# Kernel tuning notes

Hardware: AMD Instinct MI355X
Metric: run time of the kernel (lower is better)

The kernel has to match this reference:

```python
import jax, jax.numpy as jnp
import numpy as np

C1 = 0.01 ** 2
C2 = 0.03 ** 2
IN_CH = 3
WIN = 11
LEVELS = 5


def _gauss_kernel(k=WIN, sigma=1.5, c=IN_CH):
    ax = np.arange(k, dtype=np.float32) - (k - 1) / 2.0
    g = np.exp(-(ax ** 2) / (2.0 * sigma ** 2))
    g = g / g.sum()
    w2d = np.outer(g, g).astype(np.float32)  # [k,k]
    return jnp.asarray(np.tile(w2d[None, None], (c, 1, 1, 1)))  # [C,1,k,k]


def _dwconv(x, w):
    # depthwise (grouped) conv, 'same' padding for odd kernel
    pad = (w.shape[-1] - 1) // 2
    return jax.lax.conv_general_dilated(
        x, w, window_strides=(1, 1), padding=[(pad, pad), (pad, pad)],
        feature_group_count=x.shape[1],
        dimension_numbers=("NCHW", "OIHW", "NCHW"))


def _ssim_loss(i1, i2, w):
    m1 = _dwconv(i1, w)
    m2 = _dwconv(i2, w)
    m1sq = m1 * m1
    m2sq = m2 * m2
    m12 = m1 * m2
    s1 = _dwconv(i1 * i1, w) - m1sq
    s2 = _dwconv(i2 * i2, w) - m2sq
    s12 = _dwconv(i1 * i2, w) - m12
    ssim = (2 * m12 + C1) * (2 * s12 + C2) / ((m1sq + m2sq + C1) * (s1 + s2 + C2))
    return 1.0 - ssim.mean()


def _avg_pool2(x):
    B, C, H, W = x.shape
    return x.reshape(B, C, H // 2, 2, W // 2, 2).mean(axis=(3, 5))


def setup_inputs() -> dict:
    key = jax.random.key(0)
    k1, k2 = jax.random.split(key)
    img1 = jax.random.uniform(k1, (16, IN_CH, 512, 512), dtype=jnp.float32)
    img2 = jax.random.uniform(k2, (16, IN_CH, 512, 512), dtype=jnp.float32)
    inp = {"img1": img1, "img2": img2}
    for i in range(LEVELS):
        inp[f"g{i}"] = _gauss_kernel()
    return inp


def reference(img1, img2, g0, g1, g2, g3, g4):
    loss = jnp.asarray(0.0, dtype=img1.dtype)
    for w in (g0, g1, g2, g3, g4):
        loss = loss + _ssim_loss(img1, img2, w)
        img1 = _avg_pool2(img1)
        img2 = _avg_pool2(img2)
    return loss
```

## Files before the change

kernel.cpp:

```cpp
#include <hip/hip_runtime.h>
#include <math.h>

#define WIN 11
#define PAD 5
#define TW 64

typedef float v2f __attribute__((ext_vector_type(2)));

struct GW { float g[WIN]; };

template<bool EMIT>
__device__ __forceinline__ float ssim_wave_tile(
    const float* __restrict__ p1, const float* __restrict__ p2,
    int W, int X0, int Y0, const GW& gw, float2* __restrict__ rb,
    float* __restrict__ o1a, float* __restrict__ o1b, int Wout)
{
    const int TH = 32;
    const int lane = threadIdx.x & 63;
    const int gx = X0 + lane;
    const bool cval = gx < W;
    const int hx   = (lane < 5) ? (X0 - 5 + lane) : (X0 + 59 + lane);
    const bool hval = (lane < 10) && ((unsigned)hx < (unsigned)W);
    const int hpos = (lane < 5) ? lane : (64 + lane);
    const int cpos = 5 + lane;
    const int gxc = cval ? gx : 0;
    const int hxc = hval ? hx : gxc;
    const int wpos = (lane < 10) ? hpos : cpos;

    float vMp[11], vSp[11], vMq[11], vSq[11];
#pragma unroll
    for (int k = 0; k < 11; ++k) { vMp[k] = 0.f; vSp[k] = 0.f; vMq[k] = 0.f; vSq[k] = 0.f; }

    float part = 0.f;
    float pprev = 0.f, qprev = 0.f;

    auto LOAD = [&](int t, float& oa, float& ob, float& oah, float& obh) {
        int y = Y0 - PAD + t;
        bool yin = (unsigned)y < (unsigned)W;
        const float* r1 = p1 + (size_t)(yin ? y : 0) * W;
        const float* r2 = p2 + (size_t)(yin ? y : 0) * W;
        float va = r1[gxc], vb = r2[gxc];
        float wa = r1[hxc], wb = r2[hxc];
        bool cv = yin && cval;
        bool hv = yin && hval;
        oa  = cv ? va : 0.f;
        ob  = cv ? vb : 0.f;
        oah = hv ? wa : 0.f;
        obh = hv ? wb : 0.f;
    };

    float a0, b0, ah0, bh0;
    float a1, b1, ah1, bh1;
    LOAD(0, a0, b0, ah0, bh0);
    LOAD(1, a1, b1, ah1, bh1);

#pragma unroll 1
    for (int blk = 0; blk < 4; ++blk) {
#pragma unroll
        for (int u = 0; u < 11; ++u) {
            const int t = blk * 11 + u;

            float a2, b2, ah2, bh2;
            LOAD(t + 2, a2, b2, ah2, bh2);

            float p = a0 + b0, q = a0 - b0;
            float ph = ah0 + bh0, qh = ah0 - bh0;
            rb[cpos] = make_float2(p, q);
            rb[wpos] = (lane < 10) ? make_float2(ph, qh) : make_float2(p, q);
            __builtin_amdgcn_wave_barrier();

            v2f hM = {0.f, 0.f}, hS = {0.f, 0.f};
#pragma unroll
            for (int j = 0; j < WIN; ++j) {
                float2 v = rb[lane + j];
                v2f vm = { v.x, v.y };
                v2f g2 = { gw.g[j], gw.g[j] };
                hM = __builtin_elementwise_fma(g2, vm, hM);
                hS = __builtin_elementwise_fma(g2, vm * vm, hS);
            }
            __builtin_amdgcn_wave_barrier();
            float hp = hM.x, hq = hM.y, hpp = hS.x, hqq = hS.y;

#pragma unroll
            for (int s = 0; s < 11; ++s) {
                const int widx = 10 - ((s - u + 11) % 11);
                float g = gw.g[widx];
                vMp[s] = fmaf(g, hp,  vMp[s]);
                vSp[s] = fmaf(g, hpp, vSp[s]);
                vMq[s] = fmaf(g, hq,  vMq[s]);
                vSq[s] = fmaf(g, hqq, vSq[s]);
            }

            if (EMIT) {
                if (t >= 6 && t <= TH + 4 && (t & 1) == 0) {
                    float sp_ = p + pprev, sq_ = q + qprev;
                    float sp2 = sp_ + __shfl_down(sp_, 1, 64);
                    float sq2 = sq_ + __shfl_down(sq_, 1, 64);
                    if ((lane & 1) == 0) {
                        float P = sp2 * 0.25f, Q = sq2 * 0.25f;
                        int yo = (t - 6) >> 1;
                        size_t oo = (size_t)((Y0 >> 1) + yo) * Wout + ((X0 >> 1) + (lane >> 1));
                        o1a[oo] = (P + Q) * 0.5f;
                        o1b[oo] = (P - Q) * 0.5f;
                    }
                }
                pprev = p; qprev = q;
            }

            {
                int o = t - 10;
                if ((unsigned)o < (unsigned)TH) {
                    bool yok = (unsigned)(Y0 + o) < (unsigned)W;
                    float Mp = vMp[u], Sp_ = vSp[u], Mq = vMq[u], Sq_ = vSq[u];
                    const float C1v = 1e-4f, C2v = 9e-4f;
                    float A = Mp * Mp, B = Mq * Mq;
                    float ABp = A + B, ABm = A - B;
                    float SSp = Sp_ + Sq_, SSm = Sp_ - Sq_;
                    float n1 = fmaf(0.5f, ABm, C1v);
                    float n2 = fmaf(0.5f, SSm - ABm, C2v);
                    float e1 = fmaf(0.5f, ABp, C1v);
                    float e2 = fmaf(0.5f, SSp - ABp, C2v);
                    float v = (n1 * n2) * __builtin_amdgcn_rcpf(e1 * e2);
                    part += (cval && yok) ? v : 0.f;
                }
                vMp[u] = 0.f; vSp[u] = 0.f; vMq[u] = 0.f; vSq[u] = 0.f;
            }

            a0 = a1; b0 = b1; ah0 = ah1; bh0 = bh1;
            a1 = a2; b1 = b2; ah1 = ah2; bh1 = bh2;

            __builtin_amdgcn_sched_barrier(0);
        }
    }

    return part;
}

__global__ __launch_bounds__(256, 4) void ssim_l0_kernel(
    const float* __restrict__ i1, const float* __restrict__ i2,
    float* __restrict__ a1, float* __restrict__ b1,
    double* __restrict__ acc, GW gw)
{
    __shared__ float2 rbs[4][80];
    const int wid = threadIdx.x >> 6;
    const int w = blockIdx.x * 4 + wid;
    const int img = w >> 7;
    const int tt = w & 127;
    const int tx = tt & 7, ty = tt >> 3;
    const size_t off  = (size_t)img * 512 * 512;
    const size_t ooff = (size_t)img * 256 * 256;

    float part = ssim_wave_tile<true>(i1 + off, i2 + off, 512, tx * 64, ty * 32,
                                      gw, rbs[wid], a1 + ooff, b1 + ooff, 256);
#pragma unroll
    for (int o = 32; o > 0; o >>= 1) part += __shfl_down(part, o, 64);
    if ((threadIdx.x & 63) == 0) atomicAdd(acc, (double)part);
}

__global__ __launch_bounds__(256, 4) void ssim_rest_kernel(
    const float* __restrict__ a1, const float* __restrict__ b1,
    const float* __restrict__ a2, const float* __restrict__ b2,
    const float* __restrict__ a3, const float* __restrict__ b3,
    const float* __restrict__ a4, const float* __restrict__ b4,
    double* __restrict__ acc, GW gw)
{
    __shared__ float2 rbs[4][80];
    const int wid = threadIdx.x >> 6;
    const int w = blockIdx.x * 4 + wid;
    const int img = w / 43;
    const int r = w - img * 43;
    int lvl, tx, ty;
    if (r < 32)      { lvl = 1; tx = r & 3;  ty = r >> 2; }
    else if (r < 40) { lvl = 2; int s = r - 32; tx = s & 1; ty = s >> 1; }
    else if (r < 42) { lvl = 3; tx = 0; ty = r - 40; }
    else             { lvl = 4; tx = 0; ty = 0; }
    const int W = 512 >> lvl;
    const float* p1; const float* p2;
    switch (lvl) {
      case 1:  p1 = a1; p2 = b1; break;
      case 2:  p1 = a2; p2 = b2; break;
      case 3:  p1 = a3; p2 = b3; break;
      default: p1 = a4; p2 = b4; break;
    }
    const size_t off = (size_t)img * W * W;

    float part = ssim_wave_tile<false>(p1 + off, p2 + off, W, tx * 64, ty * 32,
                                       gw, rbs[wid], nullptr, nullptr, 0);
#pragma unroll
    for (int o = 32; o > 0; o >>= 1) part += __shfl_down(part, o, 64);
    if ((threadIdx.x & 63) == 0) atomicAdd(acc + lvl, (double)part);
}

__global__ __launch_bounds__(256) void pool_rest_kernel(
    const float* __restrict__ a1, const float* __restrict__ b1,
    float* __restrict__ a2, float* __restrict__ b2,
    float* __restrict__ a3, float* __restrict__ b3,
    float* __restrict__ a4, float* __restrict__ b4)
{
    __shared__ float l2[32][33];
    __shared__ float l3[16][17];
    const int tid = threadIdx.x;
    const int im = blockIdx.y;
    const int tb = blockIdx.x;
    const int tx = tb & 3, ty = tb >> 2;
    const bool second = im >= 48;
    const int ii = second ? im - 48 : im;
    const float* src = (second ? b1 : a1) + (size_t)ii * 256 * 256;
    float* o2 = (second ? b2 : a2) + (size_t)ii * 128 * 128;
    float* o3 = (second ? b3 : a3) + (size_t)ii * 64 * 64;
    float* o4 = (second ? b4 : a4) + (size_t)ii * 32 * 32;
    const int X0 = tx * 64, Y0 = ty * 64;

#pragma unroll
    for (int k = 0; k < 2; ++k) {
        int idx = tid + k * 256;
        int xp = idx & 15;
        int yo = idx >> 4;
        const float* rp = src + (size_t)(Y0 + 2 * yo) * 256 + (X0 + 4 * xp);
        float4 r0 = *(const float4*)rp;
        float4 r1 = *(const float4*)(rp + 256);
        float v0 = (r0.x + r0.y + r1.x + r1.y) * 0.25f;
        float v1 = (r0.z + r0.w + r1.z + r1.w) * 0.25f;
        l2[yo][2 * xp]     = v0;
        l2[yo][2 * xp + 1] = v1;
        float2* op = (float2*)(o2 + (size_t)((Y0 >> 1) + yo) * 128 + ((X0 >> 1) + 2 * xp));
        *op = make_float2(v0, v1);
    }
    __syncthreads();
    {
        int xo = tid & 15, yo = tid >> 4;
        if (yo < 16) {
            float v = (l2[2*yo][2*xo] + l2[2*yo][2*xo+1] +
                       l2[2*yo+1][2*xo] + l2[2*yo+1][2*xo+1]) * 0.25f;
            l3[yo][xo] = v;
            o3[(size_t)((Y0 >> 2) + yo) * 64 + ((X0 >> 2) + xo)] = v;
        }
    }
    __syncthreads();
    if (tid < 64) {
        int xo = tid & 7, yo = tid >> 3;
        float v = (l3[2*yo][2*xo] + l3[2*yo][2*xo+1] +
                   l3[2*yo+1][2*xo] + l3[2*yo+1][2*xo+1]) * 0.25f;
        o4[(size_t)((Y0 >> 3) + yo) * 32 + ((X0 >> 3) + xo)] = v;
    }
}

__global__ void final_kernel(const double* __restrict__ acc, float* __restrict__ out)
{
    double loss = 0.0;
#pragma unroll
    for (int l = 0; l < 5; ++l) {
        double cnt = 48.0 * (double)(512 >> l) * (double)(512 >> l);
        loss += 1.0 - acc[l] / cnt;
    }
    out[0] = (float)loss;
}

extern "C" void kernel_launch(void* const* d_in, const int* in_sizes, int n_in,
                              void* d_out, int out_size, void* d_ws, size_t ws_size,
                              hipStream_t stream)
{
    const float* img1 = (const float*)d_in[0];
    const float* img2 = (const float*)d_in[1];
    float* out = (float*)d_out;

    GW gw;
    double gs[WIN], sum = 0.0;
    for (int i = 0; i < WIN; ++i) {
        double ax = (double)i - 5.0;
        gs[i] = exp(-(ax * ax) / 4.5);
        sum += gs[i];
    }
    for (int i = 0; i < WIN; ++i) gw.g[i] = (float)(gs[i] / sum);

    double* acc = (double*)d_ws;
    float* base = (float*)((char*)d_ws + 64);
    const size_t n1 = 48ull * 256 * 256;
    const size_t n2 = 48ull * 128 * 128;
    const size_t n3 = 48ull * 64 * 64;
    const size_t n4 = 48ull * 32 * 32;
    float* a1 = base;      float* b1 = a1 + n1;
    float* a2 = b1 + n1;   float* b2 = a2 + n2;
    float* a3 = b2 + n2;   float* b3 = a3 + n3;
    float* a4 = b3 + n3;   float* b4 = a4 + n4;

    hipMemsetAsync(acc, 0, 5 * sizeof(double), stream);

    hipLaunchKernelGGL(ssim_l0_kernel, dim3(1536), dim3(256), 0, stream,
                       img1, img2, a1, b1, acc, gw);

    hipLaunchKernelGGL(pool_rest_kernel, dim3(16, 96), dim3(256), 0, stream,
                       a1, b1, a2, b2, a3, b3, a4, b4);

    hipLaunchKernelGGL(ssim_rest_kernel, dim3(516), dim3(256), 0, stream,
                       a1, b1, a2, b2, a3, b3, a4, b4, acc, gw);

    hipLaunchKernelGGL(final_kernel, dim3(1), dim3(1), 0, stream, acc, out);
}
```

Baseline: 263.1 us.

## Double-buffer LDS row buffer and software-pipeline horizontal pass one row ahead

Splits the per-wave LDS row buffer into two halves so the horizontal Gaussian pass for row t reads one buffer while row t+2's sums are written to the other. The LDS reads are issued at the top of the iteration, ahead of the vertical accumulation, and the global load prefetch distance grows from 2 rows to 4. The goal is to hide LDS and global load latency behind the vertical FMA chain and to drop the write-then-read barrier stall inside each row. It costs more registers (11 float2 values held live plus extra prefetch registers) and twice the shared memory per wave, which may hurt occupancy under launch_bounds(256,4).

```diff
diff --git a/kernel.cpp b/kernel.cpp
--- a/kernel.cpp
+++ b/kernel.cpp
@@ -51,35 +51,56 @@
 
     float a0, b0, ah0, bh0;
     float a1, b1, ah1, bh1;
-    LOAD(0, a0, b0, ah0, bh0);
-    LOAD(1, a1, b1, ah1, bh1);
+    float hp, hq, hpp, hqq;
+    {
+        float t0a, t0b, t0ah, t0bh;
+        float t1a, t1b, t1ah, t1bh;
+        LOAD(0, t0a, t0b, t0ah, t0bh);
+        LOAD(1, t1a, t1b, t1ah, t1bh);
+        LOAD(2, a0, b0, ah0, bh0);
+
+        float p = t0a + t0b, q = t0a - t0b;
+        float ph = t0ah + t0bh, qh = t0ah - t0bh;
+        rb[cpos] = make_float2(p, q);
+        rb[wpos] = (lane < 10) ? make_float2(ph, qh) : make_float2(p, q);
+        __builtin_amdgcn_wave_barrier();
+
+        LOAD(3, a1, b1, ah1, bh1);
+
+        v2f hM = {0.f, 0.f}, hS = {0.f, 0.f};
+#pragma unroll
+        for (int j = 0; j < WIN; ++j) {
+            float2 v = rb[lane + j];
+            v2f vm = { v.x, v.y };
+            v2f g2 = { gw.g[j], gw.g[j] };
+            hM = __builtin_elementwise_fma(g2, vm, hM);
+            hS = __builtin_elementwise_fma(g2, vm * vm, hS);
+        }
+        __builtin_amdgcn_wave_barrier();
+        hp = hM.x; hq = hM.y; hpp = hS.x; hqq = hS.y;
+
+        float p1_ = t1a + t1b, q1_ = t1a - t1b;
+        float ph1 = t1ah + t1bh, qh1 = t1ah - t1bh;
+        rb[80 + cpos] = make_float2(p1_, q1_);
+        rb[80 + wpos] = (lane < 10) ? make_float2(ph1, qh1) : make_float2(p1_, q1_);
+        __builtin_amdgcn_wave_barrier();
+        pprev = p1_; qprev = q1_;
+    }
 
 #pragma unroll 1
     for (int blk = 0; blk < 4; ++blk) {
 #pragma unroll
         for (int u = 0; u < 11; ++u) {
             const int t = blk * 11 + u;
+            const int rOff = (((blk & 1) ^ (u & 1)) ^ 1) * 80;
+            const int wOff = ((blk & 1) ^ (u & 1)) * 80;
+
+            float2 v[11];
+#pragma unroll
+            for (int j = 0; j < WIN; ++j) v[j] = rb[rOff + lane + j];
 
             float a2, b2, ah2, bh2;
-            LOAD(t + 2, a2, b2, ah2, bh2);
-
-            float p = a0 + b0, q = a0 - b0;
-            float ph = ah0 + bh0, qh = ah0 - bh0;
-            rb[cpos] = make_float2(p, q);
-            rb[wpos] = (lane < 10) ? make_float2(ph, qh) : make_float2(p, q);
-            __builtin_amdgcn_wave_barrier();
-
-            v2f hM = {0.f, 0.f}, hS = {0.f, 0.f};
-#pragma unroll
-            for (int j = 0; j < WIN; ++j) {
-                float2 v = rb[lane + j];
-                v2f vm = { v.x, v.y };
-                v2f g2 = { gw.g[j], gw.g[j] };
-                hM = __builtin_elementwise_fma(g2, vm, hM);
-                hS = __builtin_elementwise_fma(g2, vm * vm, hS);
-            }
-            __builtin_amdgcn_wave_barrier();
-            float hp = hM.x, hq = hM.y, hpp = hS.x, hqq = hS.y;
+            LOAD(t + 4, a2, b2, ah2, bh2);
 
 #pragma unroll
             for (int s = 0; s < 11; ++s) {
@@ -89,22 +110,6 @@
                 vSp[s] = fmaf(g, hpp, vSp[s]);
                 vMq[s] = fmaf(g, hq,  vMq[s]);
                 vSq[s] = fmaf(g, hqq, vSq[s]);
-            }
-
-            if (EMIT) {
-                if (t >= 6 && t <= TH + 4 && (t & 1) == 0) {
-                    float sp_ = p + pprev, sq_ = q + qprev;
-                    float sp2 = sp_ + __shfl_down(sp_, 1, 64);
-                    float sq2 = sq_ + __shfl_down(sq_, 1, 64);
-                    if ((lane & 1) == 0) {
-                        float P = sp2 * 0.25f, Q = sq2 * 0.25f;
-                        int yo = (t - 6) >> 1;
-                        size_t oo = (size_t)((Y0 >> 1) + yo) * Wout + ((X0 >> 1) + (lane >> 1));
-                        o1a[oo] = (P + Q) * 0.5f;
-                        o1b[oo] = (P - Q) * 0.5f;
-                    }
-                }
-                pprev = p; qprev = q;
             }
 
             {
@@ -120,10 +125,47 @@
                     float n2 = fmaf(0.5f, SSm - ABm, C2v);
                     float e1 = fmaf(0.5f, ABp, C1v);
                     float e2 = fmaf(0.5f, SSp - ABp, C2v);
-                    float v = (n1 * n2) * __builtin_amdgcn_rcpf(e1 * e2);
-                    part += (cval && yok) ? v : 0.f;
+                    float val = (n1 * n2) * __builtin_amdgcn_rcpf(e1 * e2);
+                    part += (cval && yok) ? val : 0.f;
                 }
                 vMp[u] = 0.f; vSp[u] = 0.f; vMq[u] = 0.f; vSq[u] = 0.f;
+            }
+
+            {
+                v2f hM = {0.f, 0.f}, hS = {0.f, 0.f};
+#pragma unroll
+                for (int j = 0; j < WIN; ++j) {
+                    v2f vm = { v[j].x, v[j].y };
+                    v2f g2 = { gw.g[j], gw.g[j] };
+                    hM = __builtin_elementwise_fma(g2, vm, hM);
+                    hS = __builtin_elementwise_fma(g2, vm * vm, hS);
+                }
+                hp = hM.x; hq = hM.y; hpp = hS.x; hqq = hS.y;
+            }
+
+            {
+                float p = a0 + b0, q = a0 - b0;
+                float ph = ah0 + bh0, qh = ah0 - bh0;
+                rb[wOff + cpos] = make_float2(p, q);
+                rb[wOff + wpos] = (lane < 10) ? make_float2(ph, qh) : make_float2(p, q);
+                __builtin_amdgcn_wave_barrier();
+
+                if (EMIT) {
+                    int r = t + 2;
+                    if (r >= 6 && r <= TH + 4 && (r & 1) == 0) {
+                        float sp_ = p + pprev, sq_ = q + qprev;
+                        float sp2 = sp_ + __shfl_down(sp_, 1, 64);
+                        float sq2 = sq_ + __shfl_down(sq_, 1, 64);
+                        if ((lane & 1) == 0) {
+                            float P = sp2 * 0.25f, Q = sq2 * 0.25f;
+                            int yo = (r - 6) >> 1;
+                            size_t oo = (size_t)((Y0 >> 1) + yo) * Wout + ((X0 >> 1) + (lane >> 1));
+                            o1a[oo] = (P + Q) * 0.5f;
+                            o1b[oo] = (P - Q) * 0.5f;
+                        }
+                    }
+                    pprev = p; qprev = q;
+                }
             }
 
             a0 = a1; b0 = b1; ah0 = ah1; bh0 = bh1;
@@ -141,7 +183,7 @@
     float* __restrict__ a1, float* __restrict__ b1,
     double* __restrict__ acc, GW gw)
 {
-    __shared__ float2 rbs[4][80];
+    __shared__ float2 rbs[4][160];
     const int wid = threadIdx.x >> 6;
     const int w = blockIdx.x * 4 + wid;
     const int img = w >> 7;
@@ -164,7 +206,7 @@
     const float* __restrict__ a4, const float* __restrict__ b4,
     double* __restrict__ acc, GW gw)
 {
-    __shared__ float2 rbs[4][80];
+    __shared__ float2 rbs[4][160];
     const int wid = threadIdx.x >> 6;
     const int w = blockIdx.x * 4 + wid;
     const int img = w / 43;
```

Result: no change. 263.2 us (+0.0%).

## Process two input rows per step with float4 LDS rows and packed vertical accumulators

Applied to the files above, without the earlier changes.

Each step of the sliding-window SSIM loop now handles two input rows. Both rows' p/q values are written into one float4 LDS slot, and the horizontal 11-tap pass reads them together, which halves the number of LDS round trips and wave barriers. The vertical accumulators become packed v2f arrays in a ring of 12 so the FMA updates can use packed instructions. This doubles the LDS buffer size, raises register pressure, and makes the emit and downsample bookkeeping more complex.

```diff
diff --git a/kernel.cpp b/kernel.cpp
--- a/kernel.cpp
+++ b/kernel.cpp
@@ -12,7 +12,7 @@
 template<bool EMIT>
 __device__ __forceinline__ float ssim_wave_tile(
     const float* __restrict__ p1, const float* __restrict__ p2,
-    int W, int X0, int Y0, const GW& gw, float2* __restrict__ rb,
+    int W, int X0, int Y0, const GW& gw, float4* __restrict__ rb,
     float* __restrict__ o1a, float* __restrict__ o1b, int Wout)
 {
     const int TH = 32;
@@ -27,9 +27,9 @@
     const int hxc = hval ? hx : gxc;
     const int wpos = (lane < 10) ? hpos : cpos;
 
-    float vMp[11], vSp[11], vMq[11], vSq[11];
-#pragma unroll
-    for (int k = 0; k < 11; ++k) { vMp[k] = 0.f; vSp[k] = 0.f; vMq[k] = 0.f; vSq[k] = 0.f; }
+    v2f vM[12], vS[12];
+#pragma unroll
+    for (int k = 0; k < 12; ++k) { vM[k] = (v2f){0.f, 0.f}; vS[k] = (v2f){0.f, 0.f}; }
 
     float part = 0.f;
     float pprev = 0.f, qprev = 0.f;
@@ -49,89 +49,120 @@
         obh = hv ? wb : 0.f;
     };
 
-    float a0, b0, ah0, bh0;
-    float a1, b1, ah1, bh1;
-    LOAD(0, a0, b0, ah0, bh0);
-    LOAD(1, a1, b1, ah1, bh1);
+    auto EMIT1 = [&](v2f M, v2f S, int o) {
+        if ((unsigned)o < (unsigned)TH) {
+            bool yok = (unsigned)(Y0 + o) < (unsigned)W;
+            float Mp = M.x, Mq = M.y, Sp_ = S.x, Sq_ = S.y;
+            const float C1v = 1e-4f, C2v = 9e-4f;
+            float A = Mp * Mp, B = Mq * Mq;
+            float ABp = A + B, ABm = A - B;
+            float SSp = Sp_ + Sq_, SSm = Sp_ - Sq_;
+            float n1 = fmaf(0.5f, ABm, C1v);
+            float n2 = fmaf(0.5f, SSm - ABm, C2v);
+            float e1 = fmaf(0.5f, ABp, C1v);
+            float e2 = fmaf(0.5f, SSp - ABp, C2v);
+            float val = (n1 * n2) * __builtin_amdgcn_rcpf(e1 * e2);
+            part += (cval && yok) ? val : 0.f;
+        }
+    };
+
+    float c0a, c0b, c0ah, c0bh, c1a, c1b, c1ah, c1bh;
+    float n0a, n0b, n0ah, n0bh, n1a, n1b, n1ah, n1bh;
+    LOAD(0, c0a, c0b, c0ah, c0bh);
+    LOAD(1, c1a, c1b, c1ah, c1bh);
+
+#define SSIM_STEP(D_, U_) do {                                                \
+    const int d_ = (D_);                                                      \
+                     \
+    LOAD(2*d_ + 2, n0a, n0b, n0ah, n0bh);                                     \
+    LOAD(2*d_ + 3, n1a, n1b, n1ah, n1bh);                                     \
+                           \
+    float p0 = c0a + c0b, q0 = c0a - c0b;                                     \
+    float p1r = c1a + c1b, q1r = c1a - c1b;                                   \
+    float ph0 = c0ah + c0bh, qh0 = c0ah - c0bh;                               \
+    float ph1 = c1ah + c1bh, qh1 = c1ah - c1bh;                               \
+    rb[cpos] = make_float4(p0, q0, p1r, q1r);                                 \
+    rb[wpos] = (lane < 10) ? make_float4(ph0, qh0, ph1, qh1)                  \
+                           : make_float4(p0, q0, p1r, q1r);                   \
+    __builtin_amdgcn_wave_barrier();    \
+                       \
+    v2f hM0 = {0.f,0.f}, hS0 = {0.f,0.f}, hM1 = {0.f,0.f}, hS1 = {0.f,0.f};  \
+    _Pragma("unroll")                                                         \
+    for (int j = 0; j < WIN; ++j) {                                           \
+        float4 vv = rb[lane + j];                                             \
+        v2f v0 = { vv.x, vv.y }, v1 = { vv.z, vv.w };                         \
+        v2f g2 = { gw.g[j], gw.g[j] };                                        \
+        hM0 = __builtin_elementwise_fma(g2, v0, hM0);                         \
+        hS0 = __builtin_elementwise_fma(g2, v0 * v0, hS0);                    \
+        hM1 = __builtin_elementwise_fma(g2, v1, hM1);                         \
+        hS1 = __builtin_elementwise_fma(g2, v1 * v1, hS1);                    \
+    }                                                                         \
+    __builtin_amdgcn_wave_barrier();   \
+                              \
+    _Pragma("unroll")                                                         \
+    for (int s = 0; s < 12; ++s) {                                            \
+        const int w0v = ((2*(U_) - s) % 12 + 12) % 12;                        \
+        if (w0v <= 10) {                                                      \
+            v2f g2 = { gw.g[w0v], gw.g[w0v] };                                \
+            vM[s] = __builtin_elementwise_fma(g2, hM0, vM[s]);                \
+            vS[s] = __builtin_elementwise_fma(g2, hS0, vS[s]);                \
+        }                                                                     \
+        const int w1v = (w0v + 1) % 12;                                       \
+        if (w1v <= 10) {                                                      \
+            v2f g2 = { gw.g[w1v], gw.g[w1v] };                                \
+            vM[s] = __builtin_elementwise_fma(g2, hM1, vM[s]);                \
+            vS[s] = __builtin_elementwise_fma(g2, hS1, vS[s]);                \
+        }                                                                     \
+    }                                                                         \
+     \
+    {                                                                         \
+        const int s0_ = (2*(U_) + 2) % 12;                                    \
+        const int s1_ = (2*(U_) + 3) % 12;                                    \
+        EMIT1(vM[s0_], vS[s0_], 2*d_ - 10);                                   \
+        EMIT1(vM[s1_], vS[s1_], 2*d_ - 9);                                    \
+        vM[s0_] = (v2f){0.f,0.f}; vS[s0_] = (v2f){0.f,0.f};                   \
+        vM[s1_] = (v2f){0.f,0.f}; vS[s1_] = (v2f){0.f,0.f};                   \
+    }                                                                         \
+                            \
+    if (EMIT) {                                                               \
+        int r_ = 2*d_;                                                        \
+        if (r_ >= 6 && r_ <= TH + 4) {                                        \
+            float sp_ = p0 + pprev, sq_ = q0 + qprev;                         \
+            float sp2 = sp_ + __shfl_down(sp_, 1, 64);                        \
+            float sq2 = sq_ + __shfl_down(sq_, 1, 64);                        \
+            if ((lane & 1) == 0) {                                            \
+                float P = sp2 * 0.25f, Q = sq2 * 0.25f;                       \
+                int yo = d_ - 3;                                              \
+                size_t oo = (size_t)((Y0 >> 1) + yo) * Wout                   \
+                          + ((X0 >> 1) + (lane >> 1));                        \
+                o1a[oo] = (P + Q) * 0.5f;                                     \
+                o1b[oo] = (P - Q) * 0.5f;                                     \
+            }                                                                 \
+        }                                                                     \
+        pprev = p1r; qprev = q1r;                                             \
+    }                                                                         \
+                                                 \
+    c0a = n0a; c0b = n0b; c0ah = n0ah; c0bh = n0bh;                           \
+    c1a = n1a; c1b = n1b; c1ah = n1ah; c1bh = n1bh;                           \
+          \
+    __builtin_amdgcn_sched_barrier(0);                                        \
+} while (0)
 
 #pragma unroll 1
-    for (int blk = 0; blk < 4; ++blk) {
-#pragma unroll
-        for (int u = 0; u < 11; ++u) {
-            const int t = blk * 11 + u;
-
-            float a2, b2, ah2, bh2;
-            LOAD(t + 2, a2, b2, ah2, bh2);
-
-            float p = a0 + b0, q = a0 - b0;
-            float ph = ah0 + bh0, qh = ah0 - bh0;
-            rb[cpos] = make_float2(p, q);
-            rb[wpos] = (lane < 10) ? make_float2(ph, qh) : make_float2(p, q);
-            __builtin_amdgcn_wave_barrier();
-
-            v2f hM = {0.f, 0.f}, hS = {0.f, 0.f};
-#pragma unroll
-            for (int j = 0; j < WIN; ++j) {
-                float2 v = rb[lane + j];
-                v2f vm = { v.x, v.y };
-                v2f g2 = { gw.g[j], gw.g[j] };
-                hM = __builtin_elementwise_fma(g2, vm, hM);
-                hS = __builtin_elementwise_fma(g2, vm * vm, hS);
-            }
-            __builtin_amdgcn_wave_barrier();
-            float hp = hM.x, hq = hM.y, hpp = hS.x, hqq = hS.y;
-
-#pragma unroll
-            for (int s = 0; s < 11; ++s) {
-                const int widx = 10 - ((s - u + 11) % 11);
-                float g = gw.g[widx];
-                vMp[s] = fmaf(g, hp,  vMp[s]);
-                vSp[s] = fmaf(g, hpp, vSp[s]);
-                vMq[s] = fmaf(g, hq,  vMq[s]);
-                vSq[s] = fmaf(g, hqq, vSq[s]);
-            }
-
-            if (EMIT) {
-                if (t >= 6 && t <= TH + 4 && (t & 1) == 0) {
-                    float sp_ = p + pprev, sq_ = q + qprev;
-                    float sp2 = sp_ + __shfl_down(sp_, 1, 64);
-                    float sq2 = sq_ + __shfl_down(sq_, 1, 64);
-                    if ((lane & 1) == 0) {
-                        float P = sp2 * 0.25f, Q = sq2 * 0.25f;
-                        int yo = (t - 6) >> 1;
-                        size_t oo = (size_t)((Y0 >> 1) + yo) * Wout + ((X0 >> 1) + (lane >> 1));
-                        o1a[oo] = (P + Q) * 0.5f;
-                        o1b[oo] = (P - Q) * 0.5f;
-                    }
-                }
-                pprev = p; qprev = q;
-            }
-
-            {
-                int o = t - 10;
-                if ((unsigned)o < (unsigned)TH) {
-                    bool yok = (unsigned)(Y0 + o) < (unsigned)W;
-                    float Mp = vMp[u], Sp_ = vSp[u], Mq = vMq[u], Sq_ = vSq[u];
-                    const float C1v = 1e-4f, C2v = 9e-4f;
-                    float A = Mp * Mp, B = Mq * Mq;
-                    float ABp = A + B, ABm = A - B;
-                    float SSp = Sp_ + Sq_, SSm = Sp_ - Sq_;
-                    float n1 = fmaf(0.5f, ABm, C1v);
-                    float n2 = fmaf(0.5f, SSm - ABm, C2v);
-                    float e1 = fmaf(0.5f, ABp, C1v);
-                    float e2 = fmaf(0.5f, SSp - ABp, C2v);
-                    float v = (n1 * n2) * __builtin_amdgcn_rcpf(e1 * e2);
-                    part += (cval && yok) ? v : 0.f;
-                }
-                vMp[u] = 0.f; vSp[u] = 0.f; vMq[u] = 0.f; vSq[u] = 0.f;
-            }
-
-            a0 = a1; b0 = b1; ah0 = ah1; bh0 = bh1;
-            a1 = a2; b1 = b2; ah1 = ah2; bh1 = bh2;
-
-            __builtin_amdgcn_sched_barrier(0);
-        }
-    }
+    for (int blk = 0; blk < 3; ++blk) {
+        const int db = blk * 6;
+        SSIM_STEP(db + 0, 0);
+        SSIM_STEP(db + 1, 1);
+        SSIM_STEP(db + 2, 2);
+        SSIM_STEP(db + 3, 3);
+        SSIM_STEP(db + 4, 4);
+        SSIM_STEP(db + 5, 5);
+    }
+    SSIM_STEP(18, 0);
+    SSIM_STEP(19, 1);
+    SSIM_STEP(20, 2);
+
+#undef SSIM_STEP
 
     return part;
 }
@@ -141,7 +172,7 @@
     float* __restrict__ a1, float* __restrict__ b1,
     double* __restrict__ acc, GW gw)
 {
-    __shared__ float2 rbs[4][80];
+    __shared__ float4 rbs[4][80];
     const int wid = threadIdx.x >> 6;
     const int w = blockIdx.x * 4 + wid;
     const int img = w >> 7;
@@ -164,7 +195,7 @@
     const float* __restrict__ a4, const float* __restrict__ b4,
     double* __restrict__ acc, GW gw)
 {
-    __shared__ float2 rbs[4][80];
+    __shared__ float4 rbs[4][80];
     const int wid = threadIdx.x >> 6;
     const int w = blockIdx.x * 4 + wid;
     const int img = w / 43;
```

Result: slower. 338.7 us (+28.7%).

## Process two input rows per step with float4 LDS staging

Applied to the files above, without the earlier changes.

Restructures the sliding-window SSIM tile loop so each step loads and horizontally filters two rows at once. Row pairs are packed into float4 LDS entries and the vertical accumulators move to a 12-slot ring with compile-time slot indices. The aim is to halve the LDS barrier/read round trips and loop overhead per row and raise ILP in the horizontal pass. In exchange it adds register pressure from extra accumulators and loaded values, and doubles LDS footprint.

```diff
diff --git a/kernel.cpp b/kernel.cpp
--- a/kernel.cpp
+++ b/kernel.cpp
@@ -3,19 +3,19 @@
 
 #define WIN 11
 #define PAD 5
-#define TW 64
 
 typedef float v2f __attribute__((ext_vector_type(2)));
 
 struct GW { float g[WIN]; };
+
+template<int N> struct IC { static constexpr int value = N; };
 
 template<bool EMIT>
 __device__ __forceinline__ float ssim_wave_tile(
     const float* __restrict__ p1, const float* __restrict__ p2,
-    int W, int X0, int Y0, const GW& gw, float2* __restrict__ rb,
+    int W, int X0, int Y0, const GW& gw, float4* __restrict__ rb,
     float* __restrict__ o1a, float* __restrict__ o1b, int Wout)
 {
-    const int TH = 32;
     const int lane = threadIdx.x & 63;
     const int gx = X0 + lane;
     const bool cval = gx < W;
@@ -27,12 +27,12 @@
     const int hxc = hval ? hx : gxc;
     const int wpos = (lane < 10) ? hpos : cpos;
 
-    float vMp[11], vSp[11], vMq[11], vSq[11];
-#pragma unroll
-    for (int k = 0; k < 11; ++k) { vMp[k] = 0.f; vSp[k] = 0.f; vMq[k] = 0.f; vSq[k] = 0.f; }
-
-    float part = 0.f;
-    float pprev = 0.f, qprev = 0.f;
+    float vMp[12], vSp[12], vMq[12], vSq[12];
+#pragma unroll
+    for (int k = 0; k < 12; ++k) { vMp[k] = 0.f; vSp[k] = 0.f; vMq[k] = 0.f; vSq[k] = 0.f; }
+
+    float part = 0.f, pprev = 0.f, qprev = 0.f;
+    float c0a, c0b, c0ah, c0bh, c1a, c1b, c1ah, c1bh;
 
     auto LOAD = [&](int t, float& oa, float& ob, float& oah, float& obh) {
         int y = Y0 - PAD + t;
@@ -49,89 +49,124 @@
         obh = hv ? wb : 0.f;
     };
 
-    float a0, b0, ah0, bh0;
-    float a1, b1, ah1, bh1;
-    LOAD(0, a0, b0, ah0, bh0);
-    LOAD(1, a1, b1, ah1, bh1);
+    auto EMIT1 = [&](float Mp, float Mq, float Sp_, float Sq_, int o) {
+        if ((unsigned)o < 32u) {
+            bool yok = (unsigned)(Y0 + o) < (unsigned)W;
+            const float C1v = 1e-4f, C2v = 9e-4f;
+            float A = Mp * Mp, B = Mq * Mq;
+            float ABp = A + B, ABm = A - B;
+            float SSp = Sp_ + Sq_, SSm = Sp_ - Sq_;
+            float n1 = fmaf(0.5f, ABm, C1v);
+            float n2 = fmaf(0.5f, SSm - ABm, C2v);
+            float e1 = fmaf(0.5f, ABp, C1v);
+            float e2 = fmaf(0.5f, SSp - ABp, C2v);
+            float val = (n1 * n2) * __builtin_amdgcn_rcpf(e1 * e2);
+            part += (cval && yok) ? val : 0.f;
+        }
+    };
+
+    LOAD(0, c0a, c0b, c0ah, c0bh);
+    LOAD(1, c1a, c1b, c1ah, c1bh);
+
+    auto step = [&](auto Uc, int d) {
+        constexpr int U = decltype(Uc)::value;
+
+        float n0, n1, n2, n3, n4, n5, n6, n7;
+        LOAD(2 * d + 2, n0, n1, n2, n3);
+        LOAD(2 * d + 3, n4, n5, n6, n7);
+
+        float p0  = c0a + c0b,  q0  = c0a - c0b;
+        float ph0 = c0ah + c0bh, qh0 = c0ah - c0bh;
+        float p1r = c1a + c1b,  q1r = c1a - c1b;
+        float ph1 = c1ah + c1bh, qh1 = c1ah - c1bh;
+        rb[cpos] = make_float4(p0, q0, p1r, q1r);
+        rb[wpos] = (lane < 10) ? make_float4(ph0, qh0, ph1, qh1)
+                               : make_float4(p0, q0, p1r, q1r);
+        __builtin_amdgcn_wave_barrier();
+
+        v2f hM0 = {0.f, 0.f}, hS0 = {0.f, 0.f};
+        v2f hM1 = {0.f, 0.f}, hS1 = {0.f, 0.f};
+#pragma unroll
+        for (int j = 0; j < WIN; ++j) {
+            float4 vv = rb[lane + j];
+            v2f v0 = { vv.x, vv.y }, v1 = { vv.z, vv.w };
+            v2f g2 = { gw.g[j], gw.g[j] };
+            hM0 = __builtin_elementwise_fma(g2, v0, hM0);
+            hS0 = __builtin_elementwise_fma(g2, v0 * v0, hS0);
+            hM1 = __builtin_elementwise_fma(g2, v1, hM1);
+            hS1 = __builtin_elementwise_fma(g2, v1 * v1, hS1);
+        }
+        __builtin_amdgcn_wave_barrier();
+        float hp0 = hM0.x, hq0 = hM0.y, hpp0 = hS0.x, hqq0 = hS0.y;
+        float hp1 = hM1.x, hq1 = hM1.y, hpp1 = hS1.x, hqq1 = hS1.y;
+
+#pragma unroll
+        for (int s = 0; s < 12; ++s) {
+            constexpr int SS = 0;  (void)SS;
+            const int w0v = ((2 * U - s) % 12 + 12) % 12;
+            if (w0v <= 10) {
+                float g = gw.g[w0v];
+                vMp[s] = fmaf(g, hp0,  vMp[s]);
+                vSp[s] = fmaf(g, hpp0, vSp[s]);
+                vMq[s] = fmaf(g, hq0,  vMq[s]);
+                vSq[s] = fmaf(g, hqq0, vSq[s]);
+            }
+            const int w1v = (w0v + 1) % 12;
+            if (w1v <= 10) {
+                float g = gw.g[w1v];
+                vMp[s] = fmaf(g, hp1,  vMp[s]);
+                vSp[s] = fmaf(g, hpp1, vSp[s]);
+                vMq[s] = fmaf(g, hq1,  vMq[s]);
+                vSq[s] = fmaf(g, hqq1, vSq[s]);
+            }
+        }
+
+        {
+            constexpr int s0 = (2 * U + 2) % 12;
+            constexpr int s1 = (2 * U + 3) % 12;
+            EMIT1(vMp[s0], vMq[s0], vSp[s0], vSq[s0], 2 * d - 10);
+            EMIT1(vMp[s1], vMq[s1], vSp[s1], vSq[s1], 2 * d - 9);
+            vMp[s0] = 0.f; vSp[s0] = 0.f; vMq[s0] = 0.f; vSq[s0] = 0.f;
+            vMp[s1] = 0.f; vSp[s1] = 0.f; vMq[s1] = 0.f; vSq[s1] = 0.f;
+        }
+
+        if (EMIT) {
+            int r_ = 2 * d;
+            if (r_ >= 6 && r_ <= 36) {
+                float sp_ = p0 + pprev, sq_ = q0 + qprev;
+                float sp2 = sp_ + __shfl_down(sp_, 1, 64);
+                float sq2 = sq_ + __shfl_down(sq_, 1, 64);
+                if ((lane & 1) == 0) {
+                    float P = sp2 * 0.25f, Q = sq2 * 0.25f;
+                    int yo = d - 3;
+                    size_t oo = (size_t)((Y0 >> 1) + yo) * Wout
+                              + ((X0 >> 1) + (lane >> 1));
+                    o1a[oo] = (P + Q) * 0.5f;
+                    o1b[oo] = (P - Q) * 0.5f;
+                }
+            }
+            pprev = p1r; qprev = q1r;
+        }
+
+        c0a = n0; c0b = n1; c0ah = n2; c0bh = n3;
+        c1a = n4; c1b = n5; c1ah = n6; c1bh = n7;
+
+        __builtin_amdgcn_sched_barrier(0);
+    };
 
 #pragma unroll 1
-    for (int blk = 0; blk < 4; ++blk) {
-#pragma unroll
-        for (int u = 0; u < 11; ++u) {
-            const int t = blk * 11 + u;
-
-            float a2, b2, ah2, bh2;
-            LOAD(t + 2, a2, b2, ah2, bh2);
-
-            float p = a0 + b0, q = a0 - b0;
-            float ph = ah0 + bh0, qh = ah0 - bh0;
-            rb[cpos] = make_float2(p, q);
-            rb[wpos] = (lane < 10) ? make_float2(ph, qh) : make_float2(p, q);
-            __builtin_amdgcn_wave_barrier();
-
-            v2f hM = {0.f, 0.f}, hS = {0.f, 0.f};
-#pragma unroll
-            for (int j = 0; j < WIN; ++j) {
-                float2 v = rb[lane + j];
-                v2f vm = { v.x, v.y };
-                v2f g2 = { gw.g[j], gw.g[j] };
-                hM = __builtin_elementwise_fma(g2, vm, hM);
-                hS = __builtin_elementwise_fma(g2, vm * vm, hS);
-            }
-            __builtin_amdgcn_wave_barrier();
-            float hp = hM.x, hq = hM.y, hpp = hS.x, hqq = hS.y;
-
-#pragma unroll
-            for (int s = 0; s < 11; ++s) {
-                const int widx = 10 - ((s - u + 11) % 11);
-                float g = gw.g[widx];
-                vMp[s] = fmaf(g, hp,  vMp[s]);
-                vSp[s] = fmaf(g, hpp, vSp[s]);
-                vMq[s] = fmaf(g, hq,  vMq[s]);
-                vSq[s] = fmaf(g, hqq, vSq[s]);
-            }
-
-            if (EMIT) {
-                if (t >= 6 && t <= TH + 4 && (t & 1) == 0) {
-                    float sp_ = p + pprev, sq_ = q + qprev;
-                    float sp2 = sp_ + __shfl_down(sp_, 1, 64);
-                    float sq2 = sq_ + __shfl_down(sq_, 1, 64);
-                    if ((lane & 1) == 0) {
-                        float P = sp2 * 0.25f, Q = sq2 * 0.25f;
-                        int yo = (t - 6) >> 1;
-                        size_t oo = (size_t)((Y0 >> 1) + yo) * Wout + ((X0 >> 1) + (lane >> 1));
-                        o1a[oo] = (P + Q) * 0.5f;
-                        o1b[oo] = (P - Q) * 0.5f;
-                    }
-                }
-                pprev = p; qprev = q;
-            }
-
-            {
-                int o = t - 10;
-                if ((unsigned)o < (unsigned)TH) {
-                    bool yok = (unsigned)(Y0 + o) < (unsigned)W;
-                    float Mp = vMp[u], Sp_ = vSp[u], Mq = vMq[u], Sq_ = vSq[u];
-                    const float C1v = 1e-4f, C2v = 9e-4f;
-                    float A = Mp * Mp, B = Mq * Mq;
-                    float ABp = A + B, ABm = A - B;
-                    float SSp = Sp_ + Sq_, SSm = Sp_ - Sq_;
-                    float n1 = fmaf(0.5f, ABm, C1v);
-                    float n2 = fmaf(0.5f, SSm - ABm, C2v);
-                    float e1 = fmaf(0.5f, ABp, C1v);
-                    float e2 = fmaf(0.5f, SSp - ABp, C2v);
-                    float v = (n1 * n2) * __builtin_amdgcn_rcpf(e1 * e2);
-                    part += (cval && yok) ? v : 0.f;
-                }
-                vMp[u] = 0.f; vSp[u] = 0.f; vMq[u] = 0.f; vSq[u] = 0.f;
-            }
-
-            a0 = a1; b0 = b1; ah0 = ah1; bh0 = bh1;
-            a1 = a2; b1 = b2; ah1 = ah2; bh1 = bh2;
-
-            __builtin_amdgcn_sched_barrier(0);
-        }
-    }
+    for (int blk = 0; blk < 3; ++blk) {
+        const int db = blk * 6;
+        step(IC<0>{}, db + 0);
+        step(IC<1>{}, db + 1);
+        step(IC<2>{}, db + 2);
+        step(IC<3>{}, db + 3);
+        step(IC<4>{}, db + 4);
+        step(IC<5>{}, db + 5);
+    }
+    step(IC<0>{}, 18);
+    step(IC<1>{}, 19);
+    step(IC<2>{}, 20);
 
     return part;
 }
@@ -141,7 +176,7 @@
     float* __restrict__ a1, float* __restrict__ b1,
     double* __restrict__ acc, GW gw)
 {
-    __shared__ float2 rbs[4][80];
+    __shared__ float4 rbs[4][80];
     const int wid = threadIdx.x >> 6;
     const int w = blockIdx.x * 4 + wid;
     const int img = w >> 7;
@@ -164,7 +199,7 @@
     const float* __restrict__ a4, const float* __restrict__ b4,
     double* __restrict__ acc, GW gw)
 {
-    __shared__ float2 rbs[4][80];
+    __shared__ float4 rbs[4][80];
     const int wid = threadIdx.x >> 6;
     const int w = blockIdx.x * 4 + wid;
     const int img = w / 43;
```

After: 351.7 us. +33.7%, slower.
